# Kernel tuning notes

Hardware: AMD Instinct MI355X
Metric: run time of the kernel (lower is better)

Reference implementation:

```python
import jax, jax.numpy as jnp
import numpy as np

IN_F, ASS, OUT_F = 1024, 100000, 1024
P = 0.0005
NUM_ROUNDS = 24  # fixed replacement for the data-dependent convergence loop
TOTAL = IN_F + ASS + OUT_F


def _build_graph(seed=0):
    """Random digraph: input->assoc and assoc->(assoc|out) with prob P,
    plus guaranteed edges so the propagation_check of the original passes
    (every assoc node reachable, every output has an in-edge)."""
    rng = np.random.default_rng(seed)
    ass0, out0 = IN_F, IN_F + ASS
    n_ie = int(P * IN_F * ASS)
    ie_src = rng.integers(0, IN_F, n_ie)
    ie_dst = rng.integers(ass0, out0, n_ie)
    n_ae = int(P * ASS * (ASS + OUT_F))
    ae_src = rng.integers(ass0, out0, n_ae)
    ae_dst = rng.integers(ass0, out0 + OUT_F, n_ae)
    # guarantee reachability: assoc node j gets an in-edge from a random node < j
    g_dst = np.arange(ass0, out0)
    g_src = (rng.random(ASS) * g_dst).astype(np.int64)
    gi = g_src < IN_F
    ie_src = np.concatenate([ie_src, g_src[gi]])
    ie_dst = np.concatenate([ie_dst, g_dst[gi]])
    ae_src = np.concatenate([ae_src, g_src[~gi]])
    ae_dst = np.concatenate([ae_dst, g_dst[~gi]])
    # every output neuron gets at least one in-edge from a random assoc
    ae_src = np.concatenate([ae_src, rng.integers(ass0, out0, OUT_F)])
    ae_dst = np.concatenate([ae_dst, np.arange(out0, out0 + OUT_F)])
    return ie_src, ie_dst, ae_src, ae_dst


def setup_inputs() -> dict:
    key = jax.random.key(0)
    k1, k2, k3 = jax.random.split(key, 3)
    ie_src, ie_dst, ae_src, ae_dst = _build_graph()
    x = jax.random.normal(k1, (1, IN_F), jnp.float32)
    # nn.init.uniform_(w, -1, 1)
    input_weights = jax.random.uniform(k2, (len(ie_src),), jnp.float32, -1.0, 1.0)
    assoc_weights = jax.random.uniform(k3, (len(ae_src),), jnp.float32, -1.0, 1.0)
    return {
        'x': x,
        'input_weights': input_weights,
        'assoc_weights': assoc_weights,
        'in_edge_src': jnp.asarray(ie_src, jnp.int32),
        'in_edge_dst': jnp.asarray(ie_dst, jnp.int32),
        'ass_edge_src': jnp.asarray(ae_src, jnp.int32),
        'ass_edge_dst': jnp.asarray(ae_dst, jnp.int32),
    }


def _forward(x, input_weights, assoc_weights, in_edge_src, in_edge_dst,
             ass_edge_src, ass_edge_dst):
    idx = jnp.arange(TOTAL)
    is_assoc = (idx >= IN_F) & (idx < IN_F + ASS)
    # --- input phase: each input neuron i sends x[i]*w along its out-edges ---
    msgs = x[0][in_edge_src] * input_weights              # [E_in]
    mem = jax.ops.segment_sum(msgs, in_edge_dst, num_segments=TOTAL)
    recv = jax.ops.segment_sum(jnp.ones_like(in_edge_dst), in_edge_dst,
                               num_segments=TOTAL) > 0
    status = jnp.where(recv, 1, 0).astype(jnp.int32)      # 0=inactive,1=working,2=activated

    # --- synchronous wave propagation through associative neurons ---
    def step(carry, _):
        mem, status = carry
        fire = (status == 1) & is_assoc                    # working assoc neurons fire
        src_fire = fire[ass_edge_src]
        # forward_fn(memory, w) = activation(sum(memory)) * w  (tanh activation)
        vals = jnp.where(src_fire, jnp.tanh(mem[ass_edge_src]) * assoc_weights, 0.0)
        delta = jax.ops.segment_sum(vals, ass_edge_dst, num_segments=TOTAL)
        got = jax.ops.segment_sum(src_fire.astype(jnp.int32), ass_edge_dst,
                                  num_segments=TOTAL) > 0
        mem = jnp.where(fire, 0.0, mem) + delta            # fired neurons erase memory
        status = jnp.where(fire, 2, jnp.where(got & (status == 0), 1, status))
        return (mem, status), None

    (mem, status), _ = jax.lax.scan(step, (mem, status), None, length=NUM_ROUNDS)
    # --- output phase: Y[i] = activation(sum(memory)) * 1 ---
    return jnp.tanh(mem[IN_F + ASS:])


def reference(x, input_weights, assoc_weights, in_edge_src, in_edge_dst,
              ass_edge_src, ass_edge_dst):
    return _forward(x, input_weights, assoc_weights, in_edge_src, in_edge_dst,
                    ass_edge_src, ass_edge_dst)
```

## Files before the change

### kernel.cpp

```cpp
#include <hip/hip_runtime.h>
#include <hip/hip_cooperative_groups.h>

namespace cg = cooperative_groups;

#define IN_F 1024
#define ASS 100000
#define OUT_F 1024
#define TOTAL (IN_F + ASS + OUT_F)
#define ASS0 IN_F
#define OUT0 (IN_F + ASS)
#define NDST (ASS + OUT_F)
#define NUM_ROUNDS 24

#define BIN_SZ 512
#define BIN_SH 9
#define BIN_MK 511
#define NBINS ((NDST + BIN_SZ - 1) / BIN_SZ)
#define NCON 512
#define CON_T 1024
#define SPLIT 8
#define NBM32 3136

typedef int i4v __attribute__((ext_vector_type(4)));
typedef float f4v __attribute__((ext_vector_type(4)));
typedef unsigned int u2v __attribute__((ext_vector_type(2)));


__global__ __launch_bounds__(256) void kz(float* mem, u2v* ltv, int* flags,
                                          int* bin_cursor, int* scur,
                                          unsigned* bm, int cap, int scap) {
  int i = blockIdx.x * 256 + threadIdx.x;
  int gs = gridDim.x * 256;
  u2v init;
  init.x = 255u;
  init.y = 0u;
  for (int k = i; k < TOTAL; k += gs) {
    mem[k] = 0.f;
    ltv[k] = init;
  }
  for (int k = i; k < NBINS; k += gs) {
    bin_cursor[k] = k * cap;
    scur[k] = k * scap;
  }
  for (int k = i; k < NBM32; k += gs) bm[k] = 0u;
  if (i < 32) flags[i] = 0;
}

__global__ __launch_bounds__(256) void ki(const float* __restrict__ x,
                                          const float* __restrict__ iw,
                                          const int* __restrict__ ies,
                                          const int* __restrict__ ied, int E_in,
                                          float* mem, unsigned int* ltv_raw,
                                          unsigned* bm) {
  int e = blockIdx.x * 256 + threadIdx.x;
  if (e < E_in) {
    int d = ied[e];
    atomicAdd(&mem[d], x[ies[e]] * iw[e]);
    ltv_raw[2 * d] = 0u;
    int b = d - ASS0;
    atomicOr(&bm[b >> 5], 1u << (b & 31));
  }
}

__global__ __launch_bounds__(256) void kp(float* mem, u2v* ltv) {
  int i = blockIdx.x * 256 + threadIdx.x;
  if (i < ASS) {
    int node = ASS0 + i;
    u2v lt = ltv[node];
    if (lt.x == 0u) {
      lt.y = __float_as_uint(tanhf(mem[node]));
      ltv[node] = lt;
      mem[node] = 0.f;
    }
  }
}

__global__ __launch_bounds__(CON_T) void kc(const int* __restrict__ aes,
                                            const int* __restrict__ aed,
                                            const float* __restrict__ aw,
                                            int E_a, int* bin_cursor,
                                            u2v* __restrict__ csr) {
  __shared__ int h[2][NBINS];
  __shared__ int cur[NBINS];
  for (int b = threadIdx.x; b < 2 * NBINS; b += CON_T)
    h[b >= NBINS][b >= NBINS ? b - NBINS : b] = 0;
  __syncthreads();
  int cp = (threadIdx.x >> 6) & 1;
  const i4v* aed4 = (const i4v*)aed;
  const i4v* aes4 = (const i4v*)aes;
  const f4v* aw4 = (const f4v*)aw;
  int nv4 = E_a >> 2;
  int stride = gridDim.x * CON_T;
  for (int v = blockIdx.x * CON_T + (int)threadIdx.x; v < nv4; v += stride) {
    i4v d4 = aed4[v];
    atomicAdd(&h[cp][(d4.x - ASS0) >> BIN_SH], 1);
    atomicAdd(&h[cp][(d4.y - ASS0) >> BIN_SH], 1);
    atomicAdd(&h[cp][(d4.z - ASS0) >> BIN_SH], 1);
    atomicAdd(&h[cp][(d4.w - ASS0) >> BIN_SH], 1);
  }
  if (blockIdx.x == 0) {
    for (int e = (nv4 << 2) + (int)threadIdx.x; e < E_a; e += CON_T)
      atomicAdd(&h[cp][(aed[e] - ASS0) >> BIN_SH], 1);
  }
  __syncthreads();
  for (int b = threadIdx.x; b < NBINS; b += CON_T) {
    int c = h[0][b] + h[1][b];
    cur[b] = c ? atomicAdd(&bin_cursor[b], c) : 0;
  }
  __syncthreads();
  for (int v = blockIdx.x * CON_T + (int)threadIdx.x; v < nv4; v += stride) {
    i4v d4 = aed4[v];
    i4v s4 = __builtin_nontemporal_load(&aes4[v]);
    f4v w4 = __builtin_nontemporal_load(&aw4[v]);
#pragma unroll
    for (int j = 0; j < 4; ++j) {
      int d = d4[j] - ASS0;
      int pos = atomicAdd(&cur[d >> BIN_SH], 1);
      u2v q;
      q.x = ((unsigned)s4[j] << BIN_SH) | (unsigned)(d & BIN_MK);
      q.y = __float_as_uint(w4[j]);
      csr[pos] = q;
    }
  }
  if (blockIdx.x == 0) {
    for (int e = (nv4 << 2) + (int)threadIdx.x; e < E_a; e += CON_T) {
      int d = aed[e] - ASS0;
      int pos = atomicAdd(&cur[d >> BIN_SH], 1);
      u2v q;
      q.x = ((unsigned)aes[e] << BIN_SH) | (unsigned)(d & BIN_MK);
      q.y = __float_as_uint(aw[e]);
      csr[pos] = q;
    }
  }
}

__global__ __launch_bounds__(256) void kRe(int r, int collect, int* flags,
                                           const int* __restrict__ bin_cursor,
                                           const u2v* __restrict__ csr,
                                           const u2v* __restrict__ ltv,
                                           const unsigned* __restrict__ bm,
                                           float* __restrict__ gslice,
                                           char* __restrict__ gmask,
                                           u2v* __restrict__ ssur, int* scur,
                                           int cap, int scap) {
  if (r > 0 && flags[r] == 0) return;
  __shared__ unsigned sbm[NBM32];
  __shared__ float slice[BIN_SZ];
  __shared__ int smask[BIN_SZ];
  int tid = threadIdx.x;
  for (int k = tid; k < NBM32; k += 256) sbm[k] = bm[k];
  for (int i = tid; i < BIN_SZ; i += 256) {
    slice[i] = 0.f;
    smask[i] = 0;
  }
  __syncthreads();
  int bin = blockIdx.x >> 3;
  int sub = blockIdx.x & (SPLIT - 1);
  int e0 = bin * cap;
  int e1 = bin_cursor[bin];
  int len = e1 - e0;
  int chunk = (len + SPLIT - 1) / SPLIT;
  int s0 = e0 + sub * chunk;
  int s1 = min(s0 + chunk, e1);
  unsigned rl = (unsigned)r;
#pragma unroll 4
  for (int e = s0 + tid; e < s1; e += 256) {
    u2v q = __builtin_nontemporal_load(&csr[e]);
    int si = (int)(q.x >> BIN_SH) - ASS0;
    bool a0 = (sbm[si >> 5] >> (si & 31)) & 1u;
    if (r == 0) {
      if (a0) {
        u2v lt = ltv[q.x >> BIN_SH];
        atomicAdd(&slice[q.x & BIN_MK],
                  __uint_as_float(lt.y) * __uint_as_float(q.y));
        smask[q.x & BIN_MK] = 1;
      }
    } else if (!a0) {
      u2v lt = ltv[q.x >> BIN_SH];
      if (lt.x == rl) {
        atomicAdd(&slice[q.x & BIN_MK],
                  __uint_as_float(lt.y) * __uint_as_float(q.y));
        smask[q.x & BIN_MK] = 1;
      } else if (collect && lt.x == 255u) {
        int pos = atomicAdd(&scur[bin], 1);
        if (pos < bin * scap + scap)
          ssur[pos] = q;
        else
          flags[30] = 1;
      }
    }
  }
  __syncthreads();
  int base = blockIdx.x * BIN_SZ;
  for (int i = tid; i < BIN_SZ; i += 256) {
    gslice[base + i] = slice[i];
    gmask[base + i] = (char)smask[i];
  }
}

__global__ __launch_bounds__(512) void kRn(int r, int* flags,
                                           const float* __restrict__ gslice,
                                           const char* __restrict__ gmask,
                                           float* __restrict__ mem,
                                           u2v* __restrict__ ltv) {
  if (r > 0 && flags[r] == 0) return;
  __shared__ int newfront;
  int tid = threadIdx.x;
  int bin = blockIdx.x;
  if (tid == 0) newfront = 0;
  __syncthreads();
  float sv = 0.f;
  int mk = 0;
  int base = bin * SPLIT * BIN_SZ + tid;
#pragma unroll
  for (int s = 0; s < SPLIT; ++s) {
    sv += gslice[base + s * BIN_SZ];
    mk |= (int)gmask[base + s * BIN_SZ];
  }
  int d = bin * BIN_SZ + tid;
  if (d < NDST && mk) {
    int node = ASS0 + d;
    float nv = mem[node] + sv;
    u2v lt = ltv[node];
    if (lt.x == 255u) {
      u2v nl;
      nl.x = (unsigned)(r + 1);
      if (node < OUT0) {
        nl.y = __float_as_uint(tanhf(nv));
        ltv[node] = nl;
        mem[node] = 0.f;
        newfront = 1;
      } else {
        nl.y = 0u;
        ltv[node] = nl;
        mem[node] = nv;
      }
    } else {
      mem[node] = nv;
    }
  }
  __syncthreads();
  if (tid == 0 && newfront) flags[r + 1] = 1;
}

__global__ __launch_bounds__(1024) void kTail(
    int* flags, const int* __restrict__ bin_cursor,
    const u2v* __restrict__ csr, const u2v* __restrict__ ssur,
    const int* __restrict__ scur, float* __restrict__ mem,
    u2v* __restrict__ ltv, float* __restrict__ out, int cap, int scap) {
  cg::grid_group g = cg::this_grid();
  __shared__ float slice[BIN_SZ];
  __shared__ int smask[BIN_SZ];
  __shared__ int newfront;
  int tid = threadIdx.x;
  int bin = blockIdx.x;
  bool useS = (flags[30] == 0);
  int e0 = useS ? bin * scap : bin * cap;
  int e1 = useS ? min(scur[bin], bin * scap + scap) : bin_cursor[bin];
  const u2v* E = useS ? ssur : csr;
  for (int r = 2; r < NUM_ROUNDS; ++r) {
    if (flags[r] == 0) break;
    if (tid < BIN_SZ) {
      slice[tid] = 0.f;
      smask[tid] = 0;
    }
    if (tid == 0) newfront = 0;
    __syncthreads();
    unsigned rl = (unsigned)r;
    for (int e = e0 + tid; e < e1; e += 1024) {
      u2v q = E[e];
      u2v lt = ltv[q.x >> BIN_SH];
      if (lt.x == rl) {
        atomicAdd(&slice[q.x & BIN_MK],
                  __uint_as_float(lt.y) * __uint_as_float(q.y));
        smask[q.x & BIN_MK] = 1;
      }
    }
    __syncthreads();
    if (tid < BIN_SZ) {
      int d = bin * BIN_SZ + tid;
      if (d < NDST && smask[tid]) {
        int node = ASS0 + d;
        float nv = mem[node] + slice[tid];
        u2v lt = ltv[node];
        if (lt.x == 255u) {
          u2v nl;
          nl.x = (unsigned)(r + 1);
          if (node < OUT0) {
            nl.y = __float_as_uint(tanhf(nv));
            ltv[node] = nl;
            mem[node] = 0.f;
            newfront = 1;
          } else {
            nl.y = 0u;
            ltv[node] = nl;
            mem[node] = nv;
          }
        } else {
          mem[node] = nv;
        }
      }
    }
    __syncthreads();
    if (tid == 0 && newfront) flags[r + 1] = 1;
    g.sync();
  }
  if (tid < BIN_SZ) {
    int d = bin * BIN_SZ + tid;
    int node = ASS0 + d;
    if (d < NDST && node >= OUT0) out[node - OUT0] = tanhf(mem[node]);
  }
}

__global__ __launch_bounds__(256) void ko(const float* __restrict__ mem,
                                          float* __restrict__ out) {
  int i = blockIdx.x * 256 + threadIdx.x;
  if (i < OUT_F) out[i] = tanhf(mem[OUT0 + i]);
}


__global__ __launch_bounds__(256) void k_init(float* mem, float* delta,
                                              int* status, int* got) {
  int i = blockIdx.x * 256 + threadIdx.x;
  if (i < TOTAL) {
    mem[i] = 0.f;
    delta[i] = 0.f;
    status[i] = 0;
    got[i] = 0;
  }
}
__global__ __launch_bounds__(256) void k_input(const float* __restrict__ x,
                                               const float* __restrict__ w,
                                               const int* __restrict__ src,
                                               const int* __restrict__ dst,
                                               int n, float* mem, int* got) {
  for (int e = blockIdx.x * 256 + threadIdx.x; e < n; e += gridDim.x * 256) {
    atomicAdd(&mem[dst[e]], x[src[e]] * w[e]);
    got[dst[e]] = 1;
  }
}
__global__ __launch_bounds__(256) void k_status0(int* status, int* got) {
  int i = blockIdx.x * 256 + threadIdx.x;
  if (i < TOTAL) {
    status[i] = got[i] ? 1 : 0;
    got[i] = 0;
  }
}
__global__ __launch_bounds__(256) void k_edge(const float* __restrict__ w,
                                              const int* __restrict__ src,
                                              const int* __restrict__ dst,
                                              int n,
                                              const float* __restrict__ mem,
                                              const int* __restrict__ status,
                                              float* delta, int* got) {
  for (int e = blockIdx.x * 256 + threadIdx.x; e < n; e += gridDim.x * 256) {
    int s = src[e];
    if (status[s] == 1) {
      atomicAdd(&delta[dst[e]], tanhf(mem[s]) * w[e]);
      got[dst[e]] = 1;
    }
  }
}
__global__ __launch_bounds__(256) void k_update(float* mem, float* delta,
                                                int* status, int* got) {
  int i = blockIdx.x * 256 + threadIdx.x;
  if (i < TOTAL) {
    int st = status[i];
    bool fire = (st == 1) && (i >= ASS0) && (i < OUT0);
    float d = delta[i];
    mem[i] = fire ? d : (mem[i] + d);
    status[i] = fire ? 2 : ((got[i] && st == 0) ? 1 : st);
    delta[i] = 0.f;
    got[i] = 0;
  }
}

extern "C" void kernel_launch(void* const* d_in, const int* in_sizes, int n_in,
                              void* d_out, int out_size, void* d_ws,
                              size_t ws_size, hipStream_t stream) {
  const float* x = (const float*)d_in[0];
  const float* iw = (const float*)d_in[1];
  const float* aw = (const float*)d_in[2];
  const int* ies = (const int*)d_in[3];
  const int* ied = (const int*)d_in[4];
  const int* aes = (const int*)d_in[5];
  const int* aed = (const int*)d_in[6];
  int E_in = in_sizes[1];
  int E_a = in_sizes[2];
  float* out = (float*)d_out;
  char* ws = (char*)d_ws;

  int cap = (((E_a / NBINS) * 13) / 10 + 255) & ~255;
  int scap = cap / 4;

  size_t off_csr = 0;
  size_t off_ssur = off_csr + (size_t)NBINS * cap * 8;
  size_t off_ltv = off_ssur + (size_t)NBINS * scap * 8;
  size_t off_mem = off_ltv + (size_t)TOTAL * 8;
  size_t off_bcur = off_mem + (size_t)TOTAL * 4;
  size_t off_scur = off_bcur + (size_t)NBINS * 4;
  size_t off_flags = off_scur + (size_t)NBINS * 4;
  size_t off_bm = off_flags + 32 * 4;
  size_t off_gsl = off_bm + (size_t)NBM32 * 4;
  size_t off_gmk = off_gsl + (size_t)NBINS * SPLIT * BIN_SZ * 4;
  size_t need = off_gmk + (size_t)NBINS * SPLIT * BIN_SZ;

  if (ws_size >= need) {
    u2v* csr = (u2v*)(ws + off_csr);
    u2v* ssur = (u2v*)(ws + off_ssur);
    u2v* ltv = (u2v*)(ws + off_ltv);
    float* mem = (float*)(ws + off_mem);
    int* bin_cursor = (int*)(ws + off_bcur);
    int* scur = (int*)(ws + off_scur);
    int* flags = (int*)(ws + off_flags);
    unsigned* bm = (unsigned*)(ws + off_bm);
    float* gslice = (float*)(ws + off_gsl);
    char* gmask = ws + off_gmk;

    kz<<<(TOTAL + 255) / 256, 256, 0, stream>>>(mem, ltv, flags, bin_cursor,
                                                scur, bm, cap, scap);
    ki<<<(E_in + 255) / 256, 256, 0, stream>>>(x, iw, ies, ied, E_in, mem,
                                               (unsigned int*)ltv, bm);
    kp<<<(ASS + 255) / 256, 256, 0, stream>>>(mem, ltv);
    kc<<<NCON, CON_T, 0, stream>>>(aes, aed, aw, E_a, bin_cursor, csr);

    for (int r = 0; r < 2; ++r) {
      kRe<<<NBINS * SPLIT, 256, 0, stream>>>(r, r == 1 ? 1 : 0, flags,
                                             bin_cursor, csr, ltv, bm, gslice,
                                             gmask, ssur, scur, cap, scap);
      kRn<<<NBINS, 512, 0, stream>>>(r, flags, gslice, gmask, mem, ltv);
    }
    void* targs[] = {(void*)&flags, (void*)&bin_cursor, (void*)&csr,
                     (void*)&ssur,  (void*)&scur,       (void*)&mem,
                     (void*)&ltv,   (void*)&out,        (void*)&cap,
                     (void*)&scap};
    hipLaunchCooperativeKernel((void*)kTail, dim3(NBINS), dim3(1024), targs, 0,
                               stream);
    return;
  }

  float* mem = (float*)ws;
  float* delta = mem + TOTAL;
  int* status = (int*)(delta + TOTAL);
  int* got = status + TOTAL;
  const int nodeBlocks = (TOTAL + 255) / 256;
  k_init<<<nodeBlocks, 256, 0, stream>>>(mem, delta, status, got);
  int inBlocks = (E_in + 255) / 256;
  if (inBlocks > 1024) inBlocks = 1024;
  k_input<<<inBlocks, 256, 0, stream>>>(x, iw, ies, ied, E_in, mem, got);
  k_status0<<<nodeBlocks, 256, 0, stream>>>(status, got);
  int eBlocks = (E_a + 255) / 256;
  if (eBlocks > 2048) eBlocks = 2048;
  for (int r = 0; r < NUM_ROUNDS; ++r) {
    k_edge<<<eBlocks, 256, 0, stream>>>(aw, aes, aed, E_a, mem, status, delta,
                                        got);
    k_update<<<nodeBlocks, 256, 0, stream>>>(mem, delta, status, got);
  }
  ko<<<(OUT_F + 255) / 256, 256, 0, stream>>>(mem, out);
}
```

Before: 159.4 us.

## Encode round-0 source flag in CSR entries, drop bitmap load in expansion kernel

```diff
diff --git a/kernel.cpp b/kernel.cpp
--- a/kernel.cpp
+++ b/kernel.cpp
@@ -20,6 +20,7 @@
 #define CON_T 1024
 #define SPLIT 8
 #define NBM32 3136
+#define A0FLAG 0x80000000u
 
 typedef int i4v __attribute__((ext_vector_type(4)));
 typedef float f4v __attribute__((ext_vector_type(4)));
@@ -79,19 +80,23 @@
                                             const int* __restrict__ aed,
                                             const float* __restrict__ aw,
                                             int E_a, int* bin_cursor,
+                                            const unsigned* __restrict__ bm,
                                             u2v* __restrict__ csr) {
-  __shared__ int h[2][NBINS];
+  __shared__ unsigned sbm[NBM32];
+  __shared__ int h[4][NBINS];
   __shared__ int cur[NBINS];
-  for (int b = threadIdx.x; b < 2 * NBINS; b += CON_T)
-    h[b >= NBINS][b >= NBINS ? b - NBINS : b] = 0;
-  __syncthreads();
-  int cp = (threadIdx.x >> 6) & 1;
+  for (int k = threadIdx.x; k < NBM32; k += CON_T) sbm[k] = bm[k];
+  for (int b = threadIdx.x; b < 4 * NBINS; b += CON_T) h[b / NBINS][b % NBINS] = 0;
+  __syncthreads();
+  int cp = (threadIdx.x >> 6) & 3;
   const i4v* aed4 = (const i4v*)aed;
   const i4v* aes4 = (const i4v*)aes;
   const f4v* aw4 = (const f4v*)aw;
   int nv4 = E_a >> 2;
-  int stride = gridDim.x * CON_T;
-  for (int v = blockIdx.x * CON_T + (int)threadIdx.x; v < nv4; v += stride) {
+  int chunk4 = (nv4 + NCON - 1) / NCON;
+  int v0 = blockIdx.x * chunk4;
+  int v1 = min(v0 + chunk4, nv4);
+  for (int v = v0 + (int)threadIdx.x; v < v1; v += CON_T) {
     i4v d4 = aed4[v];
     atomicAdd(&h[cp][(d4.x - ASS0) >> BIN_SH], 1);
     atomicAdd(&h[cp][(d4.y - ASS0) >> BIN_SH], 1);
@@ -104,20 +109,22 @@
   }
   __syncthreads();
   for (int b = threadIdx.x; b < NBINS; b += CON_T) {
-    int c = h[0][b] + h[1][b];
+    int c = h[0][b] + h[1][b] + h[2][b] + h[3][b];
     cur[b] = c ? atomicAdd(&bin_cursor[b], c) : 0;
   }
   __syncthreads();
-  for (int v = blockIdx.x * CON_T + (int)threadIdx.x; v < nv4; v += stride) {
+  for (int v = v0 + (int)threadIdx.x; v < v1; v += CON_T) {
     i4v d4 = aed4[v];
     i4v s4 = __builtin_nontemporal_load(&aes4[v]);
     f4v w4 = __builtin_nontemporal_load(&aw4[v]);
 #pragma unroll
     for (int j = 0; j < 4; ++j) {
       int d = d4[j] - ASS0;
+      int si = s4[j] - ASS0;
+      unsigned fl = ((sbm[si >> 5] >> (si & 31)) & 1u) ? A0FLAG : 0u;
       int pos = atomicAdd(&cur[d >> BIN_SH], 1);
       u2v q;
-      q.x = ((unsigned)s4[j] << BIN_SH) | (unsigned)(d & BIN_MK);
+      q.x = fl | ((unsigned)s4[j] << BIN_SH) | (unsigned)(d & BIN_MK);
       q.y = __float_as_uint(w4[j]);
       csr[pos] = q;
     }
@@ -125,9 +132,11 @@
   if (blockIdx.x == 0) {
     for (int e = (nv4 << 2) + (int)threadIdx.x; e < E_a; e += CON_T) {
       int d = aed[e] - ASS0;
+      int si = aes[e] - ASS0;
+      unsigned fl = ((sbm[si >> 5] >> (si & 31)) & 1u) ? A0FLAG : 0u;
       int pos = atomicAdd(&cur[d >> BIN_SH], 1);
       u2v q;
-      q.x = ((unsigned)aes[e] << BIN_SH) | (unsigned)(d & BIN_MK);
+      q.x = fl | ((unsigned)aes[e] << BIN_SH) | (unsigned)(d & BIN_MK);
       q.y = __float_as_uint(aw[e]);
       csr[pos] = q;
     }
@@ -138,17 +147,14 @@
                                            const int* __restrict__ bin_cursor,
                                            const u2v* __restrict__ csr,
                                            const u2v* __restrict__ ltv,
-                                           const unsigned* __restrict__ bm,
                                            float* __restrict__ gslice,
                                            char* __restrict__ gmask,
                                            u2v* __restrict__ ssur, int* scur,
                                            int cap, int scap) {
   if (r > 0 && flags[r] == 0) return;
-  __shared__ unsigned sbm[NBM32];
   __shared__ float slice[BIN_SZ];
   __shared__ int smask[BIN_SZ];
   int tid = threadIdx.x;
-  for (int k = tid; k < NBM32; k += 256) sbm[k] = bm[k];
   for (int i = tid; i < BIN_SZ; i += 256) {
     slice[i] = 0.f;
     smask[i] = 0;
@@ -166,16 +172,14 @@
 #pragma unroll 4
   for (int e = s0 + tid; e < s1; e += 256) {
     u2v q = __builtin_nontemporal_load(&csr[e]);
-    int si = (int)(q.x >> BIN_SH) - ASS0;
-    bool a0 = (sbm[si >> 5] >> (si & 31)) & 1u;
     if (r == 0) {
-      if (a0) {
-        u2v lt = ltv[q.x >> BIN_SH];
+      if (q.x & A0FLAG) {
+        u2v lt = ltv[(q.x & ~A0FLAG) >> BIN_SH];
         atomicAdd(&slice[q.x & BIN_MK],
                   __uint_as_float(lt.y) * __uint_as_float(q.y));
         smask[q.x & BIN_MK] = 1;
       }
-    } else if (!a0) {
+    } else if (!(q.x & A0FLAG)) {
       u2v lt = ltv[q.x >> BIN_SH];
       if (lt.x == rl) {
         atomicAdd(&slice[q.x & BIN_MK],
@@ -269,7 +273,7 @@
     unsigned rl = (unsigned)r;
     for (int e = e0 + tid; e < e1; e += 1024) {
       u2v q = E[e];
-      u2v lt = ltv[q.x >> BIN_SH];
+      u2v lt = ltv[(q.x & ~A0FLAG) >> BIN_SH];
       if (lt.x == rl) {
         atomicAdd(&slice[q.x & BIN_MK],
                   __uint_as_float(lt.y) * __uint_as_float(q.y));
@@ -422,11 +426,11 @@
     ki<<<(E_in + 255) / 256, 256, 0, stream>>>(x, iw, ies, ied, E_in, mem,
                                                (unsigned int*)ltv, bm);
     kp<<<(ASS + 255) / 256, 256, 0, stream>>>(mem, ltv);
-    kc<<<NCON, CON_T, 0, stream>>>(aes, aed, aw, E_a, bin_cursor, csr);
+    kc<<<NCON, CON_T, 0, stream>>>(aes, aed, aw, E_a, bin_cursor, bm, csr);
 
     for (int r = 0; r < 2; ++r) {
       kRe<<<NBINS * SPLIT, 256, 0, stream>>>(r, r == 1 ? 1 : 0, flags,
-                                             bin_cursor, csr, ltv, bm, gslice,
+                                             bin_cursor, csr, ltv, gslice,
                                              gmask, ssur, scur, cap, scap);
       kRn<<<NBINS, 512, 0, stream>>>(r, flags, gslice, gmask, mem, ltv);
     }
```

Result: faster. 151.4 us (-5.0%).
